# Performance work log

Hardware: AMD Instinct MI355X
Metric: run time of the kernel (lower is better)

## Reference

```python
import jax, jax.numpy as jnp
import numpy as np
import itertools

# Per-group attribute cardinalities (product = number of prototypes per group)
GROUP_DIMS = {
    "gender": [2],
    "hair": [5, 3],
    "top": [8, 5],
    "pants": [8, 5],
    "shoes": [6, 4],
}
TAU = 0.07  # softmax temperature for prototype similarity
B, D = 32768, 512


def _affinity(dims):
    # Faithful to _build_group_affinity: A[i,j] = fraction of matching sub-attribute values
    combos = np.array(list(itertools.product(*[range(d) for d in dims])), dtype=np.int32)  # [K, n_attrs]
    mat = (combos[:, None, :] == combos[None, :, :]).mean(-1).astype(np.float32)  # [K, K]
    return jnp.asarray(mat)


def _l2(v):
    return v / (jnp.linalg.norm(v, axis=-1, keepdims=True) + 1e-6)


def setup_inputs() -> dict:
    key = jax.random.key(0)
    ks = jax.random.split(key, 1 + len(GROUP_DIMS))
    inp = {"x": jax.random.normal(ks[0], (B, D), dtype=jnp.float32)}
    for k, (name, dims) in zip(ks[1:], GROUP_DIMS.items()):
        K = int(np.prod(dims))
        # matches nn.Parameter(torch.randn(K, D) * 0.01)
        inp[f"P_{name}"] = jax.random.normal(k, (K, D), dtype=jnp.float32) * 0.01
    return inp


def reference(x, P_gender, P_hair, P_top, P_pants, P_shoes):
    protos = {"gender": P_gender, "hair": P_hair, "top": P_top, "pants": P_pants, "shoes": P_shoes}
    xn = _l2(x)  # [B, D]
    outs = []
    for name, P in protos.items():
        A = _affinity(GROUP_DIMS[name])          # [K, K] constant affinity buffer
        logits = (xn @ _l2(P).T) / TAU           # [B, K] cosine-similarity prototype lookup
        q = jax.nn.softmax(logits, axis=-1)      # soft assignment
        q_aff = q @ A                            # affinity-weighted assignment
        q_aff = q_aff / (q_aff.sum(-1, keepdims=True) + 1e-6)
        outs.append(q_aff @ P)                   # [B, D] affinity-smoothed quantized feature
    return jnp.stack(outs, axis=1)               # [B, n_groups, D]
```

## Files before the change

### kernel.cpp

```cpp
#include <hip/hip_runtime.h>
#include <hip/hip_bf16.h>
#include <math.h>


constexpr int D    = 512;
constexpr int KTOT = 121;
constexpr float TAU = 0.07f;

constexpr int GB[5]  = {0, 2, 17, 57, 97};
constexpr int GK[5]  = {2, 15, 40, 40, 24};
constexpr int GD2[5] = {1, 3, 5, 5, 4};
constexpr int GNA[5] = {1, 2, 2, 2, 2};
constexpr int KS0[5] = {0, 0, 0, 1, 3};
constexpr int KS1[5] = {1, 1, 2, 4, 4};

using f32x4 = __attribute__((ext_vector_type(4))) float;
using s16x8 = __attribute__((ext_vector_type(8))) short;

__device__ __forceinline__ const float* pick(int k,
    const float* P0, const float* P1, const float* P2, const float* P3, const float* P4,
    int* kl) {
  if (k < 2)  { *kl = k;      return P0; }
  if (k < 17) { *kl = k - 2;  return P1; }
  if (k < 57) { *kl = k - 17; return P2; }
  if (k < 97) { *kl = k - 57; return P3; }
  *kl = k - 97; return P4;
}

__device__ __forceinline__ short f2bf(float f) {
  __hip_bfloat16 h = __float2bfloat16(f);
  return *reinterpret_cast<short*>(&h);
}

__global__ void prep_norms(const float* __restrict__ P0, const float* __restrict__ P1,
                           const float* __restrict__ P2, const float* __restrict__ P3,
                           const float* __restrict__ P4, float* __restrict__ invn) {
  int k = blockIdx.x;
  int kl; const float* P = pick(k, P0, P1, P2, P3, P4, &kl);
  const float* row = P + (size_t)kl * D;
  float s = 0.f;
  for (int d = threadIdx.x; d < D; d += 64) { float v = row[d]; s += v * v; }
  #pragma unroll
  for (int m = 1; m < 64; m <<= 1) s += __shfl_xor(s, m);
  if (threadIdx.x == 0) invn[k] = 1.f / (sqrtf(s) + 1e-6f);
}

__global__ void prep_pnbf(const float* __restrict__ P0, const float* __restrict__ P1,
                          const float* __restrict__ P2, const float* __restrict__ P3,
                          const float* __restrict__ P4, const float* __restrict__ invn,
                          unsigned short* __restrict__ pnbf) {
  int idx = blockIdx.x * 256 + threadIdx.x;
  int blk = idx >> 9, e = idx & 511;
  int lane = e >> 3, j = e & 7;
  int ct = blk >> 4, s = blk & 15;
  int col = ct * 16 + (lane & 15);
  int k   = s * 32 + (lane >> 4) * 8 + j;
  float v = 0.f;
  if (col < KTOT) {
    int kl; const float* P = pick(col, P0, P1, P2, P3, P4, &kl);
    v = P[(size_t)kl * D + k] * invn[col];
  }
  pnbf[idx] = (unsigned short)f2bf(v);
}

__global__ void prep_mptbf(const float* __restrict__ P0, const float* __restrict__ P1,
                           const float* __restrict__ P2, const float* __restrict__ P3,
                           const float* __restrict__ P4, unsigned short* __restrict__ mptbf) {
  int idx = blockIdx.x * 256 + threadIdx.x;
  int blk = idx >> 9, e = idx & 511;
  int lane = e >> 3, j = e & 7;
  int c = blk >> 2, ks = blk & 3;
  int gd = c * 16 + (lane & 15);
  int k  = ks * 32 + (lane >> 4) * 8 + j;
  int g = gd >> 9, d = gd & (D - 1);
  float v = 0.f;
  if (k >= GB[g] && k < GB[g] + GK[g]) {
    int kl = k - GB[g];
    const float* P = (g == 0) ? P0 : (g == 1) ? P1 : (g == 2) ? P2 : (g == 3) ? P3 : P4;
    int d2 = GD2[g], na = GNA[g], K = GK[g];
    int a1 = kl / d2, a2 = kl % d2;
    float s = 0.f, m = 0.f;
    for (int jj = 0; jj < K; jj++) {
      float aff;
      if (na == 1) {
        aff = (jj == kl) ? 1.f : 0.f;
      } else {
        int b1 = jj / d2, b2 = jj % d2;
        aff = 0.5f * (float)((a1 == b1) + (a2 == b2));
      }
      s += aff;
      m += aff * P[(size_t)jj * D + d];
    }
    v = m / (s + 1e-6f);
  }
  mptbf[idx] = (unsigned short)f2bf(v);
}

template <int G>
__device__ __forceinline__ void phase2_group(
    const s16x8 (&af2)[4], const unsigned short* __restrict__ mptbf,
    float* __restrict__ ob, float* __restrict__ obase, int ch, int lane) {
  const int l15 = lane & 15, hi = lane >> 4;
  #pragma unroll 1
  for (int i = 0; i < 4; ++i) {
    const int s = G * 8 + i * 2 + ch;
    const unsigned short* bp = mptbf + (size_t)(s * 4) * 4 * 512 + lane * 8;
    f32x4 a0 = (f32x4){0.f, 0.f, 0.f, 0.f}, a1 = a0, a2 = a0, a3 = a0;
    #pragma unroll
    for (int ks = KS0[G]; ks < KS1[G]; ++ks) {
      s16x8 b0 = *(const s16x8*)(bp + (0 * 4 + ks) * 512);
      s16x8 b1 = *(const s16x8*)(bp + (1 * 4 + ks) * 512);
      s16x8 b2 = *(const s16x8*)(bp + (2 * 4 + ks) * 512);
      s16x8 b3 = *(const s16x8*)(bp + (3 * 4 + ks) * 512);
      a0 = __builtin_amdgcn_mfma_f32_16x16x32_bf16(af2[ks], b0, a0, 0, 0, 0);
      a1 = __builtin_amdgcn_mfma_f32_16x16x32_bf16(af2[ks], b1, a1, 0, 0, 0);
      a2 = __builtin_amdgcn_mfma_f32_16x16x32_bf16(af2[ks], b2, a2, 0, 0, 0);
      a3 = __builtin_amdgcn_mfma_f32_16x16x32_bf16(af2[ks], b3, a3, 0, 0, 0);
    }
    #pragma unroll
    for (int j = 0; j < 4; ++j) {
      const int row = hi * 4 + j;
      ob[row * 68 +  0 + l15] = a0[j];
      ob[row * 68 + 16 + l15] = a1[j];
      ob[row * 68 + 32 + l15] = a2[j];
      ob[row * 68 + 48 + l15] = a3[j];
    }
    float* gp = obase + (size_t)s * 64 + l15 * 4;
    #pragma unroll
    for (int i2 = 0; i2 < 4; ++i2) {
      const int row = i2 * 4 + hi;
      float4 v = *(float4*)&ob[row * 68 + l15 * 4];
      *(float4*)(gp + (size_t)row * (5 * D)) = v;
    }
  }
}

__global__ __launch_bounds__(512, 4) void fused_main(
    const float* __restrict__ x, const unsigned short* __restrict__ pnbf,
    const unsigned short* __restrict__ mptbf, float* __restrict__ out) {
  __shared__ __align__(16) float smem[8704];
  __shared__ float xsqs[64];
  float (*lred)[65] = (float (*)[65])smem;

  const int tid  = threadIdx.x;
  const int lane = tid & 63;
  const int w    = __builtin_amdgcn_readfirstlane(tid >> 6);
  const int r0   = blockIdx.x * 64;

  const int wr = (w & 3) << 4;
  const int ch = w >> 2;
  const int ko = (lane >> 4) << 3;

  {
    const int arow = wr + (lane & 15);
    const float* xrow = x + (size_t)(r0 + arow) * D + ko;

    f32x4 acc[4];
    #pragma unroll
    for (int t = 0; t < 4; ++t) acc[t] = (f32x4){0.f, 0.f, 0.f, 0.f};
    float xsq = 0.f;

    #pragma unroll 4
    for (int s = 0; s < 16; ++s) {
      float4 a0 = *(const float4*)(xrow + s * 32);
      float4 a1 = *(const float4*)(xrow + s * 32 + 4);
      xsq += a0.x * a0.x + a0.y * a0.y + a0.z * a0.z + a0.w * a0.w
           + a1.x * a1.x + a1.y * a1.y + a1.z * a1.z + a1.w * a1.w;
      s16x8 af;
      af[0] = f2bf(a0.x); af[1] = f2bf(a0.y); af[2] = f2bf(a0.z); af[3] = f2bf(a0.w);
      af[4] = f2bf(a1.x); af[5] = f2bf(a1.y); af[6] = f2bf(a1.z); af[7] = f2bf(a1.w);
      #pragma unroll
      for (int t = 0; t < 4; ++t) {
        s16x8 bfv = *(const s16x8*)(pnbf + (size_t)(((ch << 2) + t) * 16 + s) * 512 + lane * 8);
        acc[t] = __builtin_amdgcn_mfma_f32_16x16x32_bf16(af, bfv, acc[t], 0, 0, 0);
      }
    }

    xsq += __shfl_xor(xsq, 16);
    xsq += __shfl_xor(xsq, 32);
    if (w < 4 && lane < 16) xsqs[wr + lane] = xsq;

    const int drow = wr + ((lane >> 4) << 2);
    #pragma unroll
    for (int t = 0; t < 4; ++t) {
      const int col = (ch << 6) + (t << 4) + (lane & 15);
      #pragma unroll
      for (int j = 0; j < 4; ++j) lred[col][drow + j] = acc[t][j];
    }
  }
  __syncthreads();

  if (w < 5) {
    const int g = w;
    const float scale = 1.f / ((sqrtf(xsqs[lane]) + 1e-6f) * TAU);
    float mx = -1e30f;
    for (int kk = 0; kk < GK[g]; ++kk)
      mx = fmaxf(mx, lred[GB[g] + kk][lane]);
    float E = 0.f;
    for (int kk = 0; kk < GK[g]; ++kk) {
      float e = __expf((lred[GB[g] + kk][lane] - mx) * scale);
      lred[GB[g] + kk][lane] = e;
      E += e;
    }
    const float inv = 1.f / E;
    for (int kk = 0; kk < GK[g]; ++kk) lred[GB[g] + kk][lane] *= inv;
  }
  __syncthreads();

  s16x8 af2[4];
  {
    const int ar = wr + (lane & 15);
    #pragma unroll
    for (int s = 0; s < 4; ++s) {
      const int kbase = s * 32 + ko;
      s16x8 f;
      #pragma unroll
      for (int j = 0; j < 8; ++j) f[j] = f2bf(lred[kbase + j][ar]);
      af2[s] = f;
    }
  }
  __syncthreads();

  {
    float* ob    = smem + w * (16 * 68);
    float* obase = out + (size_t)(r0 + wr) * (5 * D);

    phase2_group<0>(af2, mptbf, ob, obase, ch, lane);
    phase2_group<1>(af2, mptbf, ob, obase, ch, lane);
    phase2_group<2>(af2, mptbf, ob, obase, ch, lane);
    phase2_group<3>(af2, mptbf, ob, obase, ch, lane);
    phase2_group<4>(af2, mptbf, ob, obase, ch, lane);
  }
}

extern "C" void kernel_launch(void* const* d_in, const int* in_sizes, int n_in,
                              void* d_out, int out_size, void* d_ws, size_t ws_size,
                              hipStream_t stream) {
  const float* x  = (const float*)d_in[0];
  const float* P0 = (const float*)d_in[1];
  const float* P1 = (const float*)d_in[2];
  const float* P2 = (const float*)d_in[3];
  const float* P3 = (const float*)d_in[4];
  const float* P4 = (const float*)d_in[5];
  float* out = (float*)d_out;

  unsigned short* pnbf  = (unsigned short*)d_ws;
  unsigned short* mptbf = pnbf + 128 * 512;
  float* invn = (float*)(mptbf + 640 * 512);

  prep_norms<<<dim3(121), dim3(64), 0, stream>>>(P0, P1, P2, P3, P4, invn);
  prep_pnbf<<<dim3(256), dim3(256), 0, stream>>>(P0, P1, P2, P3, P4, invn, pnbf);
  prep_mptbf<<<dim3(1280), dim3(256), 0, stream>>>(P0, P1, P2, P3, P4, mptbf);
  fused_main<<<dim3(512), dim3(512), 0, stream>>>(x, pnbf, mptbf, out);
}
```

Baseline: 119.0 us.

## Split fused kernel into logits kernel and output kernel via bf16 workspace

The single fused kernel is split in two. The first computes logits and softmax for 64-row tiles and writes bf16 assignment probabilities to a workspace buffer. The second kernel uses 32-row tiles across twice as many blocks, with a higher occupancy hint, to run the MFMA output GEMM and write the large output. This aims to expose more parallelism and occupancy for the store-heavy output phase, at the cost of an extra launch and a workspace round trip of 8 MB.

```diff
diff --git a/kernel.cpp b/kernel.cpp
--- a/kernel.cpp
+++ b/kernel.cpp
@@ -96,51 +96,11 @@
   mptbf[idx] = (unsigned short)f2bf(v);
 }
 
-template <int G>
-__device__ __forceinline__ void phase2_group(
-    const s16x8 (&af2)[4], const unsigned short* __restrict__ mptbf,
-    float* __restrict__ ob, float* __restrict__ obase, int ch, int lane) {
-  const int l15 = lane & 15, hi = lane >> 4;
-  #pragma unroll 1
-  for (int i = 0; i < 4; ++i) {
-    const int s = G * 8 + i * 2 + ch;
-    const unsigned short* bp = mptbf + (size_t)(s * 4) * 4 * 512 + lane * 8;
-    f32x4 a0 = (f32x4){0.f, 0.f, 0.f, 0.f}, a1 = a0, a2 = a0, a3 = a0;
-    #pragma unroll
-    for (int ks = KS0[G]; ks < KS1[G]; ++ks) {
-      s16x8 b0 = *(const s16x8*)(bp + (0 * 4 + ks) * 512);
-      s16x8 b1 = *(const s16x8*)(bp + (1 * 4 + ks) * 512);
-      s16x8 b2 = *(const s16x8*)(bp + (2 * 4 + ks) * 512);
-      s16x8 b3 = *(const s16x8*)(bp + (3 * 4 + ks) * 512);
-      a0 = __builtin_amdgcn_mfma_f32_16x16x32_bf16(af2[ks], b0, a0, 0, 0, 0);
-      a1 = __builtin_amdgcn_mfma_f32_16x16x32_bf16(af2[ks], b1, a1, 0, 0, 0);
-      a2 = __builtin_amdgcn_mfma_f32_16x16x32_bf16(af2[ks], b2, a2, 0, 0, 0);
-      a3 = __builtin_amdgcn_mfma_f32_16x16x32_bf16(af2[ks], b3, a3, 0, 0, 0);
-    }
-    #pragma unroll
-    for (int j = 0; j < 4; ++j) {
-      const int row = hi * 4 + j;
-      ob[row * 68 +  0 + l15] = a0[j];
-      ob[row * 68 + 16 + l15] = a1[j];
-      ob[row * 68 + 32 + l15] = a2[j];
-      ob[row * 68 + 48 + l15] = a3[j];
-    }
-    float* gp = obase + (size_t)s * 64 + l15 * 4;
-    #pragma unroll
-    for (int i2 = 0; i2 < 4; ++i2) {
-      const int row = i2 * 4 + hi;
-      float4 v = *(float4*)&ob[row * 68 + l15 * 4];
-      *(float4*)(gp + (size_t)row * (5 * D)) = v;
-    }
-  }
-}
-
-__global__ __launch_bounds__(512, 4) void fused_main(
+__global__ __launch_bounds__(512, 4) void fused_logits(
     const float* __restrict__ x, const unsigned short* __restrict__ pnbf,
-    const unsigned short* __restrict__ mptbf, float* __restrict__ out) {
-  __shared__ __align__(16) float smem[8704];
+    unsigned short* __restrict__ cb) {
+  __shared__ float lred[128][65];
   __shared__ float xsqs[64];
-  float (*lred)[65] = (float (*)[65])smem;
 
   const int tid  = threadIdx.x;
   const int lane = tid & 63;
@@ -207,30 +167,88 @@
   }
   __syncthreads();
 
+  {
+    const int rl = tid >> 3;
+    const int kc = (tid & 7) << 4;
+    unsigned int pk[8];
+    #pragma unroll
+    for (int jj = 0; jj < 8; ++jj) {
+      unsigned int lo = (unsigned short)f2bf(lred[kc + 2 * jj][rl]);
+      unsigned int hi = (unsigned short)f2bf(lred[kc + 2 * jj + 1][rl]);
+      pk[jj] = lo | (hi << 16);
+    }
+    unsigned int* cp = (unsigned int*)(cb + (size_t)(r0 + rl) * 128 + kc);
+    *(uint4*)(cp + 0) = make_uint4(pk[0], pk[1], pk[2], pk[3]);
+    *(uint4*)(cp + 4) = make_uint4(pk[4], pk[5], pk[6], pk[7]);
+  }
+}
+
+template <int G>
+__device__ __forceinline__ void phase2_group(
+    const s16x8 (&af2)[4], const unsigned short* __restrict__ mptbf,
+    float* __restrict__ ob, float* __restrict__ obase, int wq, int lane) {
+  const int l15 = lane & 15, hi = lane >> 4;
+  #pragma unroll 1
+  for (int i = 0; i < 2; ++i) {
+    const int s = G * 8 + i * 4 + wq;
+    const unsigned short* bp = mptbf + (size_t)(s * 4) * 4 * 512 + lane * 8;
+    f32x4 a0 = (f32x4){0.f, 0.f, 0.f, 0.f}, a1 = a0, a2 = a0, a3 = a0;
+    #pragma unroll
+    for (int ks = KS0[G]; ks < KS1[G]; ++ks) {
+      s16x8 b0 = *(const s16x8*)(bp + (0 * 4 + ks) * 512);
+      s16x8 b1 = *(const s16x8*)(bp + (1 * 4 + ks) * 512);
+      s16x8 b2 = *(const s16x8*)(bp + (2 * 4 + ks) * 512);
+      s16x8 b3 = *(const s16x8*)(bp + (3 * 4 + ks) * 512);
+      a0 = __builtin_amdgcn_mfma_f32_16x16x32_bf16(af2[ks], b0, a0, 0, 0, 0);
+      a1 = __builtin_amdgcn_mfma_f32_16x16x32_bf16(af2[ks], b1, a1, 0, 0, 0);
+      a2 = __builtin_amdgcn_mfma_f32_16x16x32_bf16(af2[ks], b2, a2, 0, 0, 0);
+      a3 = __builtin_amdgcn_mfma_f32_16x16x32_bf16(af2[ks], b3, a3, 0, 0, 0);
+    }
+    #pragma unroll
+    for (int j = 0; j < 4; ++j) {
+      const int row = hi * 4 + j;
+      ob[row * 68 +  0 + l15] = a0[j];
+      ob[row * 68 + 16 + l15] = a1[j];
+      ob[row * 68 + 32 + l15] = a2[j];
+      ob[row * 68 + 48 + l15] = a3[j];
+    }
+    float* gp = obase + (size_t)s * 64 + l15 * 4;
+    #pragma unroll
+    for (int i2 = 0; i2 < 4; ++i2) {
+      const int row = i2 * 4 + hi;
+      float4 v = *(float4*)&ob[row * 68 + l15 * 4];
+      *(float4*)(gp + (size_t)row * (5 * D)) = v;
+    }
+  }
+}
+
+__global__ __launch_bounds__(512, 6) void fused_out(
+    const unsigned short* __restrict__ cb, const unsigned short* __restrict__ mptbf,
+    float* __restrict__ out) {
+  __shared__ __align__(16) float smem[8 * 16 * 68];
+
+  const int tid  = threadIdx.x;
+  const int lane = tid & 63;
+  const int w    = __builtin_amdgcn_readfirstlane(tid >> 6);
+  const int slab = w & 1;
+  const int wq   = w >> 1;
+  const int rg0  = blockIdx.x * 32 + slab * 16;
+
   s16x8 af2[4];
   {
-    const int ar = wr + (lane & 15);
-    #pragma unroll
-    for (int s = 0; s < 4; ++s) {
-      const int kbase = s * 32 + ko;
-      s16x8 f;
-      #pragma unroll
-      for (int j = 0; j < 8; ++j) f[j] = f2bf(lred[kbase + j][ar]);
-      af2[s] = f;
-    }
-  }
-  __syncthreads();
-
-  {
-    float* ob    = smem + w * (16 * 68);
-    float* obase = out + (size_t)(r0 + wr) * (5 * D);
-
-    phase2_group<0>(af2, mptbf, ob, obase, ch, lane);
-    phase2_group<1>(af2, mptbf, ob, obase, ch, lane);
-    phase2_group<2>(af2, mptbf, ob, obase, ch, lane);
-    phase2_group<3>(af2, mptbf, ob, obase, ch, lane);
-    phase2_group<4>(af2, mptbf, ob, obase, ch, lane);
-  }
+    const unsigned short* cp = cb + (size_t)(rg0 + (lane & 15)) * 128 + ((lane >> 4) << 3);
+    #pragma unroll
+    for (int ks = 0; ks < 4; ++ks) af2[ks] = *(const s16x8*)(cp + ks * 32);
+  }
+
+  float* ob    = smem + w * (16 * 68);
+  float* obase = out + (size_t)rg0 * (5 * D);
+
+  phase2_group<0>(af2, mptbf, ob, obase, wq, lane);
+  phase2_group<1>(af2, mptbf, ob, obase, wq, lane);
+  phase2_group<2>(af2, mptbf, ob, obase, wq, lane);
+  phase2_group<3>(af2, mptbf, ob, obase, wq, lane);
+  phase2_group<4>(af2, mptbf, ob, obase, wq, lane);
 }
 
 extern "C" void kernel_launch(void* const* d_in, const int* in_sizes, int n_in,
@@ -246,10 +264,12 @@
 
   unsigned short* pnbf  = (unsigned short*)d_ws;
   unsigned short* mptbf = pnbf + 128 * 512;
-  float* invn = (float*)(mptbf + 640 * 512);
+  unsigned short* cb    = mptbf + 640 * 512;
+  float* invn = (float*)(cb + (size_t)32768 * 128);
 
   prep_norms<<<dim3(121), dim3(64), 0, stream>>>(P0, P1, P2, P3, P4, invn);
   prep_pnbf<<<dim3(256), dim3(256), 0, stream>>>(P0, P1, P2, P3, P4, invn, pnbf);
   prep_mptbf<<<dim3(1280), dim3(256), 0, stream>>>(P0, P1, P2, P3, P4, mptbf);
-  fused_main<<<dim3(512), dim3(512), 0, stream>>>(x, pnbf, mptbf, out);
-}
+  fused_logits<<<dim3(512), dim3(512), 0, stream>>>(x, pnbf, cb);
+  fused_out<<<dim3(1024), dim3(512), 0, stream>>>(cb, mptbf, out);
+}
```

After: 123.5 us. 3.8% more time.
